# Performance work log

Hardware: AMD Instinct MI355X
Metric: run time of the kernel (lower is better)

Reference implementation:

```python
import jax, jax.numpy as jnp
import numpy as np

H, D, IN, E, N = 4, 16, 64, 400000, 100000
RELS = [("c1c1", "C1", "C1"), ("c1c2", "C1", "C2"), ("c1c3", "C1", "C3"),
        ("c2c1", "C2", "C1"), ("c2c2", "C2", "C2"), ("c2c3", "C2", "C3"),
        ("c3c1", "C3", "C1"), ("c3c2", "C3", "C2"), ("c3c3", "C3", "C3")]
TYPES = ("C1", "C2", "C3")


def setup_inputs() -> dict:
    key = jax.random.key(0)
    ks = iter(jax.random.split(key, 128))
    inp = {}
    for t in TYPES:
        inp["feat_" + t] = jax.random.normal(next(ks), (N, IN), jnp.float32)
        inp["W_" + t] = jax.random.normal(next(ks), (IN, H * D), jnp.float32) * 0.05
        inp["b_" + t] = jnp.zeros((H * D,), jnp.float32)
    for r, s, d in RELS:
        inp["W_" + r] = jax.random.normal(next(ks), (IN, H * D), jnp.float32) * 0.05
        inp["b_" + r] = jnp.zeros((H * D,), jnp.float32)
        inp["asrc_" + r] = jax.random.normal(next(ks), (H, D), jnp.float32) * 0.1
        inp["adst_" + r] = jax.random.normal(next(ks), (H, D), jnp.float32) * 0.1
        inp["src_" + r] = jax.random.randint(next(ks), (E,), 0, N, jnp.int32)
        inp["dst_" + r] = jax.random.randint(next(ks), (E,), 0, N, jnp.int32)
    return inp


def _forward(feats, selfp, relp):
    # leaky_relu with negative_slope = l_alpha = 0.2
    lrelu = lambda x: jnp.where(x >= 0, x, 0.2 * x)
    # per-type self projections Wh_T  [N, H, D]
    Wh_self = {t: (feats[t] @ selfp[t][0] + selfp[t][1]).reshape(-1, H, D) for t in TYPES}
    agg = {t: jnp.zeros((feats[t].shape[0], H, D), feats[t].dtype) for t in TYPES}
    for r, s, d in RELS:
        W, b, asrc, adst, src, dst = relp[r]
        # project once per source node, then gather per edge (same math as per-edge fc)
        Wh = (feats[s] @ W + b).reshape(-1, H, D)      # [Ns, H, D]
        whe = Wh[src]                                   # [E, H, D]
        # attention logits: (Wh_e * a_src).sum(-1) + (Wh_self_dst * a_dst).sum(-1)
        e = lrelu((whe * asrc).sum(-1) + (Wh_self[d][dst] * adst).sum(-1))  # [E, H]
        # nn.Softmax(dim=1) in the original acts over the heads axis of [E, H, 1]
        alpha = jax.nn.softmax(e, axis=1)[..., None]    # [E, H, 1]
        agg[d] = agg[d] + jax.ops.segment_sum(whe * alpha, dst, num_segments=agg[d].shape[0])
    return tuple(jax.nn.relu(agg[t]) for t in TYPES)


def reference(feat_C1, feat_C2, feat_C3, W_C1, b_C1, W_C2, b_C2, W_C3, b_C3,
              W_c1c1, b_c1c1, asrc_c1c1, adst_c1c1, src_c1c1, dst_c1c1,
              W_c1c2, b_c1c2, asrc_c1c2, adst_c1c2, src_c1c2, dst_c1c2,
              W_c1c3, b_c1c3, asrc_c1c3, adst_c1c3, src_c1c3, dst_c1c3,
              W_c2c1, b_c2c1, asrc_c2c1, adst_c2c1, src_c2c1, dst_c2c1,
              W_c2c2, b_c2c2, asrc_c2c2, adst_c2c2, src_c2c2, dst_c2c2,
              W_c2c3, b_c2c3, asrc_c2c3, adst_c2c3, src_c2c3, dst_c2c3,
              W_c3c1, b_c3c1, asrc_c3c1, adst_c3c1, src_c3c1, dst_c3c1,
              W_c3c2, b_c3c2, asrc_c3c2, adst_c3c2, src_c3c2, dst_c3c2,
              W_c3c3, b_c3c3, asrc_c3c3, adst_c3c3, src_c3c3, dst_c3c3):
    L = dict(locals())
    feats = {t: L["feat_" + t] for t in TYPES}
    selfp = {t: (L["W_" + t], L["b_" + t]) for t in TYPES}
    relp = {r: (L["W_" + r], L["b_" + r], L["asrc_" + r], L["adst_" + r], L["src_" + r], L["dst_" + r]) for r, _, _ in RELS}
    return _forward(feats, selfp, relp)
```

## Files before the change

kernel.cpp:

```cpp
#include <hip/hip_runtime.h>
#include <hip/hip_bf16.h>

constexpr int IN_F = 64;
constexpr int HD   = 64;

constexpr int BW_BITS = 10;
constexpr int BWIDTH  = 1 << BW_BITS;
constexpr int BCAP    = 6144;
constexpr int BIN_EPT = 16;
constexpr int BIN_CHUNK = 256 * BIN_EPT;

constexpr int PROJ_ROWS  = 128;
constexpr int LDS_STRIDE = 72;
constexpr int NJOBS      = 18;

typedef __attribute__((ext_vector_type(8))) short short8;
typedef __attribute__((ext_vector_type(4))) float floatx4;
typedef __attribute__((ext_vector_type(4))) unsigned short us4;
typedef __attribute__((ext_vector_type(8))) unsigned short us8;

static __device__ __forceinline__ float bf2f(unsigned short u) {
  union { unsigned int i; float f; } c; c.i = ((unsigned int)u) << 16; return c.f;
}
static __device__ __forceinline__ unsigned short f2bf_bits(float f) {
  union { __hip_bfloat16 h; unsigned short u; } c; c.h = __float2bfloat16(f); return c.u;
}

struct PrepParams {
  const float* W[3][4];
  const float* b[3][4];
  const float* asrc[9];
  const float* adst[9];
  unsigned short* Bpack;
  float* biasPack;
  unsigned* bcnt;
  int nbc;
};

__global__ __launch_bounds__(64) void prep_kernel(PrepParams pp) {
  const int t = blockIdx.x / NJOBS;
  const int j = blockIdx.x % NJOBS;
  const int lane = threadIdx.x;
  const int q = lane >> 4, n = lane & 15;

  {
    const int gid = blockIdx.x * 64 + lane;
    if (gid < pp.nbc) pp.bcnt[gid] = 0u;
  }

  const float* W; const float* bv; const float* av = nullptr;
  int n0 = 0; bool dotjob;
  if (j < 3) {
    W = pp.W[t][0]; bv = pp.b[t][0]; av = pp.adst[j * 3 + t]; dotjob = true;
  } else {
    const int jj = j - 3, p = jj / 5, sub = jj % 5;
    W = pp.W[t][1 + p]; bv = pp.b[t][1 + p];
    if (sub < 4) { n0 = sub * 16; dotjob = false; }
    else { av = pp.asrc[t * 3 + p]; dotjob = true; }
  }

  unsigned short* outB = pp.Bpack + (size_t)(t * NJOBS + j) * 2 * 64 * 8;
  for (int kt = 0; kt < 2; ++kt) {
    for (int jj = 0; jj < 8; ++jj) {
      const int k = kt * 32 + q * 8 + jj;
      float v = 0.f;
      if (!dotjob) v = W[k * 64 + n0 + n];
      else if (n < 4) {
        for (int d = 0; d < 16; ++d) v += W[k * 64 + n * 16 + d] * av[n * 16 + d];
      }
      outB[(kt * 64 + lane) * 8 + jj] = f2bf_bits(v);
    }
  }
  if (lane < 16) {
    float v = 0.f;
    if (!dotjob) v = bv[n0 + lane];
    else if (lane < 4) {
      for (int d = 0; d < 16; ++d) v += bv[lane * 16 + d] * av[lane * 16 + d];
    }
    pp.biasPack[(t * NJOBS + j) * 16 + lane] = v;
  }
}

struct ProjParams {
  const float* feat[3];
  const unsigned short* Bpack;
  const float* biasPack;
  unsigned short* wh[9];
  float* sdot[9];
  float* ddot[9];
  int N;
};

static __device__ __forceinline__ void proj_body(const ProjParams& p, int bx, int t,
                                                 unsigned short* featL) {
  const int n0blk = bx * PROJ_ROWS;
  const int tid = threadIdx.x;
  const int N = p.N;

  {
    const float* feat = p.feat[t];
    #pragma unroll
    for (int c = 0; c < 8; ++c) {
      const int flat = c * 256 + tid;
      const int row = flat >> 4;
      const int c4  = (flat & 15) << 2;
      const int gr = n0blk + row;
      float4 v = make_float4(0.f, 0.f, 0.f, 0.f);
      if (gr < N) v = *(const float4*)(feat + (size_t)gr * IN_F + c4);
      ushort4 o;
      o.x = f2bf_bits(v.x); o.y = f2bf_bits(v.y);
      o.z = f2bf_bits(v.z); o.w = f2bf_bits(v.w);
      *(ushort4*)(featL + row * LDS_STRIDE + c4) = o;
    }
  }
  __syncthreads();

  const int wave = tid >> 6;
  const int lane = tid & 63;
  const int q = lane >> 4, l15 = lane & 15;

  short8 afrag[2][2];
  #pragma unroll
  for (int mt = 0; mt < 2; ++mt) {
    const int row = wave * 32 + mt * 16 + l15;
    #pragma unroll
    for (int kt = 0; kt < 2; ++kt) {
      afrag[mt][kt] = *(const short8*)(featL + row * LDS_STRIDE + kt * 32 + q * 8);
    }
  }
  __syncthreads();

  const unsigned short* Bbase = p.Bpack + (size_t)t * NJOBS * 2 * 64 * 8;
  const float* biasBase = p.biasPack + (size_t)t * NJOBS * 16;

  short8 b0 = *(const short8*)(Bbase + 0 * 512 + lane * 8);
  short8 b1 = *(const short8*)(Bbase + 1 * 512 + lane * 8);
  float bias = biasBase[l15];

  for (int j = 0; j < NJOBS; ++j) {
    short8 b0n, b1n; float biasn = 0.f;
    if (j + 1 < NJOBS) {
      b0n = *(const short8*)(Bbase + ((size_t)(j + 1) * 2 + 0) * 512 + lane * 8);
      b1n = *(const short8*)(Bbase + ((size_t)(j + 1) * 2 + 1) * 512 + lane * 8);
      biasn = biasBase[(j + 1) * 16 + l15];
    }

    #pragma unroll
    for (int mt = 0; mt < 2; ++mt) {
      floatx4 acc = {bias, bias, bias, bias};
      acc = __builtin_amdgcn_mfma_f32_16x16x32_bf16(afrag[mt][0], b0, acc, 0, 0, 0);
      acc = __builtin_amdgcn_mfma_f32_16x16x32_bf16(afrag[mt][1], b1, acc, 0, 0, 0);
      const int lrbase = wave * 32 + mt * 16 + q * 4;
      if (j < 3) {
        if (l15 < 4) {
          float* dp = p.ddot[j * 3 + t];
          #pragma unroll
          for (int r = 0; r < 4; ++r) {
            const int gr = n0blk + lrbase + r;
            if (gr < N) dp[(size_t)gr * 4 + l15] = acc[r];
          }
        }
      } else {
        const int jj = j - 3, pidx = jj / 5, sub = jj % 5, ri = t * 3 + pidx;
        if (sub < 4) {
          #pragma unroll
          for (int r = 0; r < 4; ++r) {
            featL[(lrbase + r) * LDS_STRIDE + sub * 16 + l15] = f2bf_bits(acc[r]);
          }
        } else if (l15 < 4) {
          float* sp = p.sdot[ri];
          #pragma unroll
          for (int r = 0; r < 4; ++r) {
            const int gr = n0blk + lrbase + r;
            if (gr < N) sp[(size_t)gr * 4 + l15] = acc[r];
          }
        }
      }
    }

    if (j >= 3 && ((j - 3) % 5) == 3) {
      const int ri = t * 3 + (j - 3) / 5;
      unsigned short* whp = p.wh[ri];
      const int lr = wave * 32 + (lane >> 1);
      const int gr = n0blk + lr;
      const int c0 = (lane & 1) * 32;
      if (gr < N) {
        #pragma unroll
        for (int k2 = 0; k2 < 4; ++k2) {
          us8 v = *(const us8*)(featL + lr * LDS_STRIDE + c0 + k2 * 8);
          *(us8*)(whp + (size_t)gr * HD + c0 + k2 * 8) = v;
        }
      }
    }

    b0 = b0n; b1 = b1n; bias = biasn;
  }
}

struct EdgeLists { const int* src[9]; const int* dst[9]; int E; int N; };

static __device__ __forceinline__ void bin_body(const EdgeLists& el, unsigned* bcnt,
                                                unsigned* binBuf, int nbuck,
                                                int bx, int r, unsigned* ldsu) {
  unsigned* bh    = ldsu;
  unsigned* bcur  = ldsu + 128;
  unsigned* bbase = ldsu + 256;
  const int tid = threadIdx.x;
  const int e0  = bx * BIN_CHUNK;
  const int E   = el.E;
  const int* srcp = el.src[r];
  const int* dstp = el.dst[r];

  if (tid < 128) { bh[tid] = 0u; bcur[tid] = 0u; }
  __syncthreads();

  int sv[BIN_EPT], dv[BIN_EPT];
  #pragma unroll
  for (int i = 0; i < BIN_EPT; ++i) {
    const int e = e0 + i * 256 + tid;
    if (e < E) {
      sv[i] = srcp[e];
      dv[i] = dstp[e];
      atomicAdd(&bh[dv[i] >> BW_BITS], 1u);
    } else dv[i] = -1;
  }
  __syncthreads();

  if (tid < 128) {
    bbase[tid] = (tid < nbuck && bh[tid] > 0u)
                   ? atomicAdd(bcnt + (size_t)r * nbuck + tid, bh[tid]) : 0u;
  }
  __syncthreads();

  unsigned* bb = binBuf + (size_t)r * nbuck * BCAP;
  #pragma unroll
  for (int i = 0; i < BIN_EPT; ++i) {
    if (dv[i] >= 0) {
      const int b = dv[i] >> BW_BITS;
      const unsigned pos = bbase[b] + atomicAdd(&bcur[b], 1u);
      if (pos < (unsigned)BCAP)
        bb[(size_t)b * BCAP + pos] = (unsigned)sv[i] | ((unsigned)(dv[i] & (BWIDTH - 1)) << 17);
    }
  }
}

struct FusedParams {
  ProjParams proj;
  EdgeLists el;
  unsigned* bcnt;
  unsigned* binBuf;
  int nbuck;
  int projNB;
  int binNB;
};

__global__ __launch_bounds__(256) void fused_kernel(FusedParams fp) {
  __shared__ unsigned short ldsBuf[PROJ_ROWS * LDS_STRIDE];
  const int projTotal = fp.projNB * 3;
  const int bid = (int)blockIdx.x;
  if (bid < projTotal) {
    proj_body(fp.proj, bid % fp.projNB, bid / fp.projNB, ldsBuf);
  } else {
    const int b2 = bid - projTotal;
    bin_body(fp.el, fp.bcnt, fp.binBuf, fp.nbuck,
             b2 % fp.binNB, b2 / fp.binNB, (unsigned*)ldsBuf);
  }
}

struct CsrParams {
  const unsigned* binBuf;
  const unsigned* bcnt;
  unsigned* offsets;
  unsigned* perm;
  unsigned short* alf;
  const float* sdot[9];
  const float* ddot[9];
  int N, E, nbuck;
};

__global__ __launch_bounds__(256) void csr_kernel(CsrParams cp) {
  const int r   = blockIdx.y;
  const int b   = blockIdx.x;
  const int tid = threadIdx.x;
  const int N = cp.N, E = cp.E, nbuck = cp.nbuck;
  const unsigned* bcr = cp.bcnt + (size_t)r * nbuck;
  unsigned* offr = cp.offsets + (size_t)r * (N + 1);
  unsigned* permr = cp.perm + (size_t)r * E;
  unsigned short* alfr = cp.alf + (size_t)r * E * 4;
  const float* sdr = cp.sdot[r];
  const float* ddr = cp.ddot[r];

  __shared__ unsigned S[BWIDTH];
  __shared__ unsigned T[256];
  __shared__ unsigned permL[BCAP];

  unsigned pre = (tid < b) ? bcr[tid] : 0u;
  if (pre > (unsigned)BCAP) pre = BCAP;
  pre += __shfl_xor(pre, 1);  pre += __shfl_xor(pre, 2);
  pre += __shfl_xor(pre, 4);  pre += __shfl_xor(pre, 8);
  pre += __shfl_xor(pre, 16); pre += __shfl_xor(pre, 32);
  if ((tid & 63) == 0) T[tid >> 6] = pre;
  unsigned cnt = bcr[b];
  if (cnt > (unsigned)BCAP) cnt = BCAP;
  __syncthreads();
  const unsigned base = T[0] + T[1] + T[2] + T[3];
  __syncthreads();

  const unsigned* buf = cp.binBuf + ((size_t)r * nbuck + b) * BCAP;

  for (int i = tid; i < BWIDTH; i += 256) S[i] = 0u;
  __syncthreads();

  for (unsigned i = tid; i < cnt; i += 256) atomicAdd(&S[buf[i] >> 17], 1u);
  __syncthreads();

  const int b4 = tid * 4;
  unsigned loc0 = S[b4], loc1 = S[b4 + 1], loc2 = S[b4 + 2], loc3 = S[b4 + 3];
  unsigned s = loc0 + loc1 + loc2 + loc3;
  T[tid] = s;
  __syncthreads();
  for (int d = 1; d < 256; d <<= 1) {
    const unsigned v = T[tid];
    const unsigned a = (tid >= d) ? T[tid - d] : 0u;
    __syncthreads();
    T[tid] = v + a;
    __syncthreads();
  }
  unsigned run = T[tid] - s;
  S[b4]     = run;  run += loc0;
  S[b4 + 1] = run;  run += loc1;
  S[b4 + 2] = run;  run += loc2;
  S[b4 + 3] = run;
  __syncthreads();

  const int d0 = b * BWIDTH;
  for (int i = tid; i < BWIDTH; i += 256) {
    const int d = d0 + i;
    if (d < N) offr[d] = base + S[i];
  }
  if (b == 0 && tid == 0) offr[N] = (unsigned)E;
  __syncthreads();

  for (unsigned i = tid; i < cnt; i += 256) {
    const unsigned v = buf[i];
    const unsigned pos = atomicAdd(&S[v >> 17], 1u);
    permL[pos] = v;
  }
  __syncthreads();

  for (unsigned i = tid; i < cnt; i += 256) {
    const unsigned v = permL[i];
    const unsigned sv = v & 0x1FFFFu;
    const int dn = d0 + (int)(v >> 17);
    permr[base + i] = sv;

    const float4 sd = *(const float4*)(sdr + (size_t)sv * 4);
    const float4 dd = *(const float4*)(ddr + (size_t)dn * 4);
    float e0 = sd.x + dd.x, e1 = sd.y + dd.y, e2 = sd.z + dd.z, e3 = sd.w + dd.w;
    e0 = (e0 >= 0.f) ? e0 : 0.2f * e0;
    e1 = (e1 >= 0.f) ? e1 : 0.2f * e1;
    e2 = (e2 >= 0.f) ? e2 : 0.2f * e2;
    e3 = (e3 >= 0.f) ? e3 : 0.2f * e3;
    const float m = fmaxf(fmaxf(e0, e1), fmaxf(e2, e3));
    const float x0 = __expf(e0 - m);
    const float x1 = __expf(e1 - m);
    const float x2 = __expf(e2 - m);
    const float x3 = __expf(e3 - m);
    const float inv = 1.f / (x0 + x1 + x2 + x3);
    uint2 packed;
    packed.x = ((unsigned)f2bf_bits(x1 * inv) << 16) | f2bf_bits(x0 * inv);
    packed.y = ((unsigned)f2bf_bits(x3 * inv) << 16) | f2bf_bits(x2 * inv);
    *(uint2*)(alfr + (size_t)(base + i) * 4) = packed;
  }
}

struct AggParams {
  const unsigned* offsets[9];
  const unsigned* perm[9];
  const unsigned short* alf[9];
  const unsigned short* wh[9];
  float* outp[3];
  int N, E;
};

__global__ __launch_bounds__(256) void agg_kernel(AggParams p, int t) {
  const int w    = threadIdx.x >> 6;
  const int lane = threadIdx.x & 63;
  const int n    = blockIdx.x * 4 + w;
  if (n >= p.N) return;
  const int slot = lane >> 3;
  const int l8   = lane & 7;
  const unsigned hb = (unsigned)((l8 >> 1) * 2);

  unsigned st[3], en[3];
  const char* __restrict__ pm[3];
  const char* __restrict__ al[3];
  const char* __restrict__ whr[3];
  #pragma unroll
  for (int sj = 0; sj < 3; ++sj) {
    const int r = sj * 3 + t;
    pm[sj]  = (const char*)p.perm[r];
    al[sj]  = (const char*)p.alf[r];
    whr[sj] = (const char*)p.wh[r];
    st[sj]  = p.offsets[r][n];
    en[sj]  = p.offsets[r][n + 1];
  }

  float acc[8];
  #pragma unroll
  for (int k = 0; k < 8; ++k) acc[k] = 0.f;

  unsigned sv[3]; float a[3];
  #pragma unroll
  for (int sj = 0; sj < 3; ++sj) {
    const unsigned s = st[sj], e = en[sj];
    const unsigned pos = s + (unsigned)slot;
    const unsigned pc  = (e > s) ? ((pos < e) ? pos : e - 1) : 0u;
    sv[sj] = *(const unsigned*)(pm[sj] + pc * 4u);
    a[sj]  = (pos < e) ? bf2f(*(const unsigned short*)(al[sj] + pc * 8u + hb)) : 0.f;
  }

  us8 wv[3];
  #pragma unroll
  for (int sj = 0; sj < 3; ++sj) {
    wv[sj] = *(const us8*)(whr[sj] + sv[sj] * 128u + (unsigned)(l8 * 16));
  }

  #pragma unroll
  for (int sj = 0; sj < 3; ++sj) {
    #pragma unroll
    for (int k = 0; k < 8; ++k) {
      acc[k] = fmaf(a[sj], bf2f(wv[sj][k]), acc[k]);
    }
  }

  #pragma unroll
  for (int sj = 0; sj < 3; ++sj) {
    const unsigned e = en[sj];
    for (unsigned bse = st[sj] + 8; bse < e; bse += 8) {
      const unsigned pos  = bse + (unsigned)slot;
      const unsigned posc = (pos < e) ? pos : e - 1;
      const unsigned s2 = *(const unsigned*)(pm[sj] + posc * 4u);
      const float a2 = (pos < e) ? bf2f(*(const unsigned short*)(al[sj] + posc * 8u + hb)) : 0.f;
      const us8 wv2 = *(const us8*)(whr[sj] + s2 * 128u + (unsigned)(l8 * 16));
      #pragma unroll
      for (int k = 0; k < 8; ++k) {
        acc[k] = fmaf(a2, bf2f(wv2[k]), acc[k]);
      }
    }
  }

  #pragma unroll
  for (int k = 0; k < 8; ++k) {
    acc[k] += __shfl_xor(acc[k], 8);
    acc[k] += __shfl_xor(acc[k], 16);
    acc[k] += __shfl_xor(acc[k], 32);
  }

  if (slot == 0) {
    float4 v0, v1;
    v0.x = fmaxf(acc[0], 0.f); v0.y = fmaxf(acc[1], 0.f);
    v0.z = fmaxf(acc[2], 0.f); v0.w = fmaxf(acc[3], 0.f);
    v1.x = fmaxf(acc[4], 0.f); v1.y = fmaxf(acc[5], 0.f);
    v1.z = fmaxf(acc[6], 0.f); v1.w = fmaxf(acc[7], 0.f);
    float* op = p.outp[t] + (size_t)n * HD + l8 * 8;
    *(float4*)(op) = v0;
    *(float4*)(op + 4) = v1;
  }
}

extern "C" void kernel_launch(void* const* d_in, const int* in_sizes, int n_in,
                              void* d_out, int out_size, void* d_ws, size_t ws_size,
                              hipStream_t stream) {
  const int N = in_sizes[0] / IN_F;
  const int E = in_sizes[9 + 4];
  const int nbuck = (N + BWIDTH - 1) >> BW_BITS;

  FusedParams fp; AggParams ap; CsrParams cp; PrepParams qq;
  ProjParams& pp = fp.proj;
  EdgeLists& el = fp.el;
  pp.N = N; ap.N = N; ap.E = E; el.E = E; el.N = N;
  cp.N = N; cp.E = E; cp.nbuck = nbuck;

  for (int t = 0; t < 3; ++t) {
    pp.feat[t] = (const float*)d_in[t * 3 + 0];
    qq.W[t][0] = (const float*)d_in[t * 3 + 1];
    qq.b[t][0] = (const float*)d_in[t * 3 + 2];
    for (int j = 0; j < 3; ++j) {
      const int base = 9 + (t * 3 + j) * 6;
      qq.W[t][1 + j] = (const float*)d_in[base + 0];
      qq.b[t][1 + j] = (const float*)d_in[base + 1];
    }
  }

  char* ws = (char*)d_ws;
  const size_t whBytes  = (size_t)N * HD * sizeof(__hip_bfloat16);
  const size_t dotBytes = (size_t)N * 4 * sizeof(float);
  char* whBase   = ws;
  char* sdotBase = whBase + 9 * whBytes;
  char* ddotBase = sdotBase + 9 * dotBytes;
  unsigned* offsets = (unsigned*)(ddotBase + 9 * dotBytes);
  unsigned* bcnt    = offsets + (size_t)9 * (N + 1);
  unsigned* perm    = bcnt + (size_t)9 * ((nbuck + 63) & ~63);
  unsigned short* alf = (unsigned short*)(perm + (size_t)9 * E);
  unsigned* binBuf  = (unsigned*)(alf + (size_t)9 * E * 4);
  unsigned short* Bpack = (unsigned short*)(binBuf + (size_t)9 * nbuck * BCAP);
  float* biasPack = (float*)(Bpack + (size_t)3 * NJOBS * 2 * 64 * 8);

  cp.offsets = offsets; cp.perm = perm; cp.alf = alf;
  cp.binBuf = binBuf; cp.bcnt = bcnt;
  qq.Bpack = Bpack; qq.biasPack = biasPack;
  qq.bcnt = bcnt; qq.nbc = 9 * nbuck;
  pp.Bpack = Bpack; pp.biasPack = biasPack;
  fp.bcnt = bcnt; fp.binBuf = binBuf; fp.nbuck = nbuck;
  fp.projNB = (N + PROJ_ROWS - 1) / PROJ_ROWS;
  fp.binNB  = (E + BIN_CHUNK - 1) / BIN_CHUNK;

  for (int ri = 0; ri < 9; ++ri) {
    const int base = 9 + ri * 6;
    qq.asrc[ri] = (const float*)d_in[base + 2];
    qq.adst[ri] = (const float*)d_in[base + 3];
    pp.wh[ri]   = (unsigned short*)(whBase + (size_t)ri * whBytes);
    pp.sdot[ri] = (float*)(sdotBase + (size_t)ri * dotBytes);
    pp.ddot[ri] = (float*)(ddotBase + (size_t)ri * dotBytes);
    el.src[ri]  = (const int*)d_in[base + 4];
    el.dst[ri]  = (const int*)d_in[base + 5];
    cp.sdot[ri] = pp.sdot[ri];
    cp.ddot[ri] = pp.ddot[ri];
    ap.wh[ri]   = pp.wh[ri];
    ap.alf[ri]  = alf + (size_t)ri * E * 4;
    ap.offsets[ri] = offsets + (size_t)ri * (N + 1);
    ap.perm[ri]    = perm + (size_t)ri * E;
  }
  for (int t = 0; t < 3; ++t) ap.outp[t] = (float*)d_out + (size_t)t * N * HD;

  prep_kernel<<<dim3(3 * NJOBS), 64, 0, stream>>>(qq);

  const int nblk = fp.projNB * 3 + fp.binNB * 9;
  fused_kernel<<<dim3(nblk), 256, 0, stream>>>(fp);

  csr_kernel<<<dim3(nbuck, 9), 256, 0, stream>>>(cp);

  for (int t = 0; t < 3; ++t)
    agg_kernel<<<dim3((N + 3) / 4), 256, 0, stream>>>(ap, t);
}
```

Measured before the change: 557.2 us.

## Replace CSR build and per-node aggregation with bucketed LDS-atomic aggregation

Destination buckets shrink to 64 nodes and are shared by the three relations that feed each destination type. The relation index is packed into the binned edge word. A new fab kernel computes the per-edge head softmax and accumulates alpha-weighted projected features into a shared-memory tile with LDS float atomics, then writes the ReLU output. This drops the CSR offset/permutation pass, the global perm and alpha buffers, and three separate aggregation launches. In exchange it relies on LDS atomics and a fixed per-bucket capacity of 1280 edges, which silently drops any overflow.

```diff
diff --git a/kernel.cpp b/kernel.cpp
--- a/kernel.cpp
+++ b/kernel.cpp
@@ -4,11 +4,12 @@
 constexpr int IN_F = 64;
 constexpr int HD   = 64;
 
-constexpr int BW_BITS = 10;
+constexpr int BW_BITS = 6;
 constexpr int BWIDTH  = 1 << BW_BITS;
-constexpr int BCAP    = 6144;
+constexpr int FBCAP   = 1280;
 constexpr int BIN_EPT = 16;
 constexpr int BIN_CHUNK = 256 * BIN_EPT;
+constexpr int ACC_PAD  = 66;
 
 constexpr int PROJ_ROWS  = 128;
 constexpr int LDS_STRIDE = 72;
@@ -16,7 +17,6 @@
 
 typedef __attribute__((ext_vector_type(8))) short short8;
 typedef __attribute__((ext_vector_type(4))) float floatx4;
-typedef __attribute__((ext_vector_type(4))) unsigned short us4;
 typedef __attribute__((ext_vector_type(8))) unsigned short us8;
 
 static __device__ __forceinline__ float bf2f(unsigned short u) {
@@ -43,10 +43,8 @@
   const int lane = threadIdx.x;
   const int q = lane >> 4, n = lane & 15;
 
-  {
-    const int gid = blockIdx.x * 64 + lane;
-    if (gid < pp.nbc) pp.bcnt[gid] = 0u;
-  }
+  for (int gid = blockIdx.x * 64 + lane; gid < pp.nbc; gid += 64 * gridDim.x)
+    pp.bcnt[gid] = 0u;
 
   const float* W; const float* bv; const float* av = nullptr;
   int n0 = 0; bool dotjob;
@@ -201,17 +199,19 @@
 
 static __device__ __forceinline__ void bin_body(const EdgeLists& el, unsigned* bcnt,
                                                 unsigned* binBuf, int nbuck,
-                                                int bx, int r, unsigned* ldsu) {
+                                                int bx, int ri, unsigned* ldsu) {
   unsigned* bh    = ldsu;
-  unsigned* bcur  = ldsu + 128;
-  unsigned* bbase = ldsu + 256;
+  unsigned* bcur  = ldsu + nbuck;
+  unsigned* bbase = ldsu + 2 * nbuck;
   const int tid = threadIdx.x;
   const int e0  = bx * BIN_CHUNK;
   const int E   = el.E;
-  const int* srcp = el.src[r];
-  const int* dstp = el.dst[r];
-
-  if (tid < 128) { bh[tid] = 0u; bcur[tid] = 0u; }
+  const int tt  = ri % 3;
+  const int sj  = ri / 3;
+  const int* srcp = el.src[ri];
+  const int* dstp = el.dst[ri];
+
+  for (int i = tid; i < nbuck; i += 256) { bh[i] = 0u; bcur[i] = 0u; }
   __syncthreads();
 
   int sv[BIN_EPT], dv[BIN_EPT];
@@ -226,20 +226,22 @@
   }
   __syncthreads();
 
-  if (tid < 128) {
-    bbase[tid] = (tid < nbuck && bh[tid] > 0u)
-                   ? atomicAdd(bcnt + (size_t)r * nbuck + tid, bh[tid]) : 0u;
-  }
-  __syncthreads();
-
-  unsigned* bb = binBuf + (size_t)r * nbuck * BCAP;
+  for (int i = tid; i < nbuck; i += 256) {
+    bbase[i] = (bh[i] > 0u)
+                 ? atomicAdd(bcnt + (size_t)tt * nbuck + i, bh[i]) : 0u;
+  }
+  __syncthreads();
+
+  unsigned* bb = binBuf + (size_t)tt * nbuck * FBCAP;
   #pragma unroll
   for (int i = 0; i < BIN_EPT; ++i) {
     if (dv[i] >= 0) {
       const int b = dv[i] >> BW_BITS;
       const unsigned pos = bbase[b] + atomicAdd(&bcur[b], 1u);
-      if (pos < (unsigned)BCAP)
-        bb[(size_t)b * BCAP + pos] = (unsigned)sv[i] | ((unsigned)(dv[i] & (BWIDTH - 1)) << 17);
+      if (pos < (unsigned)FBCAP)
+        bb[(size_t)b * FBCAP + pos] =
+          (unsigned)sv[i] | ((unsigned)(dv[i] & (BWIDTH - 1)) << 17)
+                          | ((unsigned)sj << 23);
     }
   }
 }
@@ -255,217 +257,118 @@
 };
 
 __global__ __launch_bounds__(256) void fused_kernel(FusedParams fp) {
-  __shared__ unsigned short ldsBuf[PROJ_ROWS * LDS_STRIDE];
+  __shared__ unsigned ldsU[4704];
   const int projTotal = fp.projNB * 3;
   const int bid = (int)blockIdx.x;
   if (bid < projTotal) {
-    proj_body(fp.proj, bid % fp.projNB, bid / fp.projNB, ldsBuf);
+    proj_body(fp.proj, bid % fp.projNB, bid / fp.projNB, (unsigned short*)ldsU);
   } else {
     const int b2 = bid - projTotal;
     bin_body(fp.el, fp.bcnt, fp.binBuf, fp.nbuck,
-             b2 % fp.binNB, b2 / fp.binNB, (unsigned*)ldsBuf);
-  }
-}
-
-struct CsrParams {
+             b2 % fp.binNB, b2 / fp.binNB, ldsU);
+  }
+}
+
+struct FabParams {
+  const unsigned* bcnt;
   const unsigned* binBuf;
-  const unsigned* bcnt;
-  unsigned* offsets;
-  unsigned* perm;
-  unsigned short* alf;
   const float* sdot[9];
   const float* ddot[9];
-  int N, E, nbuck;
-};
-
-__global__ __launch_bounds__(256) void csr_kernel(CsrParams cp) {
-  const int r   = blockIdx.y;
-  const int b   = blockIdx.x;
-  const int tid = threadIdx.x;
-  const int N = cp.N, E = cp.E, nbuck = cp.nbuck;
-  const unsigned* bcr = cp.bcnt + (size_t)r * nbuck;
-  unsigned* offr = cp.offsets + (size_t)r * (N + 1);
-  unsigned* permr = cp.perm + (size_t)r * E;
-  unsigned short* alfr = cp.alf + (size_t)r * E * 4;
-  const float* sdr = cp.sdot[r];
-  const float* ddr = cp.ddot[r];
-
-  __shared__ unsigned S[BWIDTH];
-  __shared__ unsigned T[256];
-  __shared__ unsigned permL[BCAP];
-
-  unsigned pre = (tid < b) ? bcr[tid] : 0u;
-  if (pre > (unsigned)BCAP) pre = BCAP;
-  pre += __shfl_xor(pre, 1);  pre += __shfl_xor(pre, 2);
-  pre += __shfl_xor(pre, 4);  pre += __shfl_xor(pre, 8);
-  pre += __shfl_xor(pre, 16); pre += __shfl_xor(pre, 32);
-  if ((tid & 63) == 0) T[tid >> 6] = pre;
-  unsigned cnt = bcr[b];
-  if (cnt > (unsigned)BCAP) cnt = BCAP;
-  __syncthreads();
-  const unsigned base = T[0] + T[1] + T[2] + T[3];
-  __syncthreads();
-
-  const unsigned* buf = cp.binBuf + ((size_t)r * nbuck + b) * BCAP;
-
-  for (int i = tid; i < BWIDTH; i += 256) S[i] = 0u;
-  __syncthreads();
-
-  for (unsigned i = tid; i < cnt; i += 256) atomicAdd(&S[buf[i] >> 17], 1u);
-  __syncthreads();
-
-  const int b4 = tid * 4;
-  unsigned loc0 = S[b4], loc1 = S[b4 + 1], loc2 = S[b4 + 2], loc3 = S[b4 + 3];
-  unsigned s = loc0 + loc1 + loc2 + loc3;
-  T[tid] = s;
-  __syncthreads();
-  for (int d = 1; d < 256; d <<= 1) {
-    const unsigned v = T[tid];
-    const unsigned a = (tid >= d) ? T[tid - d] : 0u;
-    __syncthreads();
-    T[tid] = v + a;
-    __syncthreads();
-  }
-  unsigned run = T[tid] - s;
-  S[b4]     = run;  run += loc0;
-  S[b4 + 1] = run;  run += loc1;
-  S[b4 + 2] = run;  run += loc2;
-  S[b4 + 3] = run;
-  __syncthreads();
-
-  const int d0 = b * BWIDTH;
-  for (int i = tid; i < BWIDTH; i += 256) {
-    const int d = d0 + i;
-    if (d < N) offr[d] = base + S[i];
-  }
-  if (b == 0 && tid == 0) offr[N] = (unsigned)E;
-  __syncthreads();
-
-  for (unsigned i = tid; i < cnt; i += 256) {
-    const unsigned v = buf[i];
-    const unsigned pos = atomicAdd(&S[v >> 17], 1u);
-    permL[pos] = v;
-  }
-  __syncthreads();
-
-  for (unsigned i = tid; i < cnt; i += 256) {
-    const unsigned v = permL[i];
-    const unsigned sv = v & 0x1FFFFu;
-    const int dn = d0 + (int)(v >> 17);
-    permr[base + i] = sv;
-
-    const float4 sd = *(const float4*)(sdr + (size_t)sv * 4);
-    const float4 dd = *(const float4*)(ddr + (size_t)dn * 4);
-    float e0 = sd.x + dd.x, e1 = sd.y + dd.y, e2 = sd.z + dd.z, e3 = sd.w + dd.w;
-    e0 = (e0 >= 0.f) ? e0 : 0.2f * e0;
-    e1 = (e1 >= 0.f) ? e1 : 0.2f * e1;
-    e2 = (e2 >= 0.f) ? e2 : 0.2f * e2;
-    e3 = (e3 >= 0.f) ? e3 : 0.2f * e3;
-    const float m = fmaxf(fmaxf(e0, e1), fmaxf(e2, e3));
-    const float x0 = __expf(e0 - m);
-    const float x1 = __expf(e1 - m);
-    const float x2 = __expf(e2 - m);
-    const float x3 = __expf(e3 - m);
-    const float inv = 1.f / (x0 + x1 + x2 + x3);
-    uint2 packed;
-    packed.x = ((unsigned)f2bf_bits(x1 * inv) << 16) | f2bf_bits(x0 * inv);
-    packed.y = ((unsigned)f2bf_bits(x3 * inv) << 16) | f2bf_bits(x2 * inv);
-    *(uint2*)(alfr + (size_t)(base + i) * 4) = packed;
-  }
-}
-
-struct AggParams {
-  const unsigned* offsets[9];
-  const unsigned* perm[9];
-  const unsigned short* alf[9];
   const unsigned short* wh[9];
   float* outp[3];
-  int N, E;
+  int N, nbuck;
 };
 
-__global__ __launch_bounds__(256) void agg_kernel(AggParams p, int t) {
-  const int w    = threadIdx.x >> 6;
-  const int lane = threadIdx.x & 63;
-  const int n    = blockIdx.x * 4 + w;
-  if (n >= p.N) return;
-  const int slot = lane >> 3;
-  const int l8   = lane & 7;
-  const unsigned hb = (unsigned)((l8 >> 1) * 2);
-
-  unsigned st[3], en[3];
-  const char* __restrict__ pm[3];
-  const char* __restrict__ al[3];
-  const char* __restrict__ whr[3];
-  #pragma unroll
-  for (int sj = 0; sj < 3; ++sj) {
-    const int r = sj * 3 + t;
-    pm[sj]  = (const char*)p.perm[r];
-    al[sj]  = (const char*)p.alf[r];
-    whr[sj] = (const char*)p.wh[r];
-    st[sj]  = p.offsets[r][n];
-    en[sj]  = p.offsets[r][n + 1];
-  }
-
-  float acc[8];
-  #pragma unroll
-  for (int k = 0; k < 8; ++k) acc[k] = 0.f;
-
-  unsigned sv[3]; float a[3];
-  #pragma unroll
-  for (int sj = 0; sj < 3; ++sj) {
-    const unsigned s = st[sj], e = en[sj];
-    const unsigned pos = s + (unsigned)slot;
-    const unsigned pc  = (e > s) ? ((pos < e) ? pos : e - 1) : 0u;
-    sv[sj] = *(const unsigned*)(pm[sj] + pc * 4u);
-    a[sj]  = (pos < e) ? bf2f(*(const unsigned short*)(al[sj] + pc * 8u + hb)) : 0.f;
-  }
-
-  us8 wv[3];
-  #pragma unroll
-  for (int sj = 0; sj < 3; ++sj) {
-    wv[sj] = *(const us8*)(whr[sj] + sv[sj] * 128u + (unsigned)(l8 * 16));
-  }
-
-  #pragma unroll
-  for (int sj = 0; sj < 3; ++sj) {
-    #pragma unroll
-    for (int k = 0; k < 8; ++k) {
-      acc[k] = fmaf(a[sj], bf2f(wv[sj][k]), acc[k]);
-    }
-  }
-
-  #pragma unroll
-  for (int sj = 0; sj < 3; ++sj) {
-    const unsigned e = en[sj];
-    for (unsigned bse = st[sj] + 8; bse < e; bse += 8) {
-      const unsigned pos  = bse + (unsigned)slot;
-      const unsigned posc = (pos < e) ? pos : e - 1;
-      const unsigned s2 = *(const unsigned*)(pm[sj] + posc * 4u);
-      const float a2 = (pos < e) ? bf2f(*(const unsigned short*)(al[sj] + posc * 8u + hb)) : 0.f;
-      const us8 wv2 = *(const us8*)(whr[sj] + s2 * 128u + (unsigned)(l8 * 16));
+__global__ __launch_bounds__(256) void fab_kernel(FabParams fb) {
+  const int t  = blockIdx.y;
+  const int b  = blockIdx.x;
+  const int d0 = b * BWIDTH;
+  const int tid = threadIdx.x;
+  const int N = fb.N;
+
+  __shared__ float accum[BWIDTH][ACC_PAD];
+  __shared__ float ddL[3][BWIDTH][4];
+  __shared__ float alphaL[256][4];
+  __shared__ unsigned wordL[256];
+
+  for (int i = tid; i < BWIDTH * ACC_PAD; i += 256)
+    (&accum[0][0])[i] = 0.f;
+  if (tid < 3 * BWIDTH) {
+    const int sj = tid >> BW_BITS, i = tid & (BWIDTH - 1);
+    const int d = d0 + i;
+    float4 v = make_float4(0.f, 0.f, 0.f, 0.f);
+    if (d < N) v = *(const float4*)(fb.ddot[sj * 3 + t] + (size_t)d * 4);
+    ddL[sj][i][0] = v.x; ddL[sj][i][1] = v.y;
+    ddL[sj][i][2] = v.z; ddL[sj][i][3] = v.w;
+  }
+  __syncthreads();
+
+  unsigned cnt = fb.bcnt[(size_t)t * fb.nbuck + b];
+  if (cnt > (unsigned)FBCAP) cnt = FBCAP;
+  const unsigned* buf = fb.binBuf + ((size_t)t * fb.nbuck + b) * FBCAP;
+
+  const int l8 = tid & 7;
+  const int eslot = tid >> 3;
+  const int h = l8 >> 1;
+
+  for (unsigned c0 = 0; c0 < cnt; c0 += 256) {
+    const unsigned lim = (cnt - c0 < 256u) ? (cnt - c0) : 256u;
+
+    if (tid < (int)lim) {
+      const unsigned v  = buf[c0 + tid];
+      const unsigned sv = v & 0x1FFFFu;
+      const unsigned dl = (v >> 17) & (BWIDTH - 1);
+      const unsigned sj = v >> 23;
+      const float4 sd = *(const float4*)(fb.sdot[sj * 3 + t] + (size_t)sv * 4);
+      float e0 = sd.x + ddL[sj][dl][0];
+      float e1 = sd.y + ddL[sj][dl][1];
+      float e2 = sd.z + ddL[sj][dl][2];
+      float e3 = sd.w + ddL[sj][dl][3];
+      e0 = (e0 >= 0.f) ? e0 : 0.2f * e0;
+      e1 = (e1 >= 0.f) ? e1 : 0.2f * e1;
+      e2 = (e2 >= 0.f) ? e2 : 0.2f * e2;
+      e3 = (e3 >= 0.f) ? e3 : 0.2f * e3;
+      const float m = fmaxf(fmaxf(e0, e1), fmaxf(e2, e3));
+      const float x0 = __expf(e0 - m);
+      const float x1 = __expf(e1 - m);
+      const float x2 = __expf(e2 - m);
+      const float x3 = __expf(e3 - m);
+      const float inv = 1.f / (x0 + x1 + x2 + x3);
+      alphaL[tid][0] = x0 * inv; alphaL[tid][1] = x1 * inv;
+      alphaL[tid][2] = x2 * inv; alphaL[tid][3] = x3 * inv;
+      wordL[tid] = v;
+    }
+    __syncthreads();
+
+    for (unsigned j = (unsigned)eslot; j < lim; j += 32) {
+      const unsigned v  = wordL[j];
+      const unsigned sv = v & 0x1FFFFu;
+      const unsigned dl = (v >> 17) & (BWIDTH - 1);
+      const unsigned sj = v >> 23;
+      const float a = alphaL[j][h];
+      const us8 wv = *(const us8*)((const char*)fb.wh[sj * 3 + t]
+                                   + sv * 128u + (unsigned)(l8 * 16));
+      float* ar = &accum[dl][l8 * 8];
       #pragma unroll
-      for (int k = 0; k < 8; ++k) {
-        acc[k] = fmaf(a2, bf2f(wv2[k]), acc[k]);
-      }
-    }
-  }
-
-  #pragma unroll
-  for (int k = 0; k < 8; ++k) {
-    acc[k] += __shfl_xor(acc[k], 8);
-    acc[k] += __shfl_xor(acc[k], 16);
-    acc[k] += __shfl_xor(acc[k], 32);
-  }
-
-  if (slot == 0) {
-    float4 v0, v1;
-    v0.x = fmaxf(acc[0], 0.f); v0.y = fmaxf(acc[1], 0.f);
-    v0.z = fmaxf(acc[2], 0.f); v0.w = fmaxf(acc[3], 0.f);
-    v1.x = fmaxf(acc[4], 0.f); v1.y = fmaxf(acc[5], 0.f);
-    v1.z = fmaxf(acc[6], 0.f); v1.w = fmaxf(acc[7], 0.f);
-    float* op = p.outp[t] + (size_t)n * HD + l8 * 8;
-    *(float4*)(op) = v0;
-    *(float4*)(op + 4) = v1;
+      for (int k = 0; k < 8; ++k)
+        atomicAdd(&ar[k], a * bf2f(wv[k]));
+    }
+    __syncthreads();
+  }
+
+  float* op = fb.outp[t];
+  for (int f4 = tid; f4 < BWIDTH * 16; f4 += 256) {
+    const int row = f4 >> 4;
+    const int c4  = (f4 & 15) << 2;
+    const int d = d0 + row;
+    if (d < N) {
+      float4 o;
+      o.x = fmaxf(accum[row][c4 + 0], 0.f);
+      o.y = fmaxf(accum[row][c4 + 1], 0.f);
+      o.z = fmaxf(accum[row][c4 + 2], 0.f);
+      o.w = fmaxf(accum[row][c4 + 3], 0.f);
+      *(float4*)(op + (size_t)d * HD + c4) = o;
+    }
   }
 }
 
@@ -476,11 +379,11 @@
   const int E = in_sizes[9 + 4];
   const int nbuck = (N + BWIDTH - 1) >> BW_BITS;
 
-  FusedParams fp; AggParams ap; CsrParams cp; PrepParams qq;
+  FusedParams fp; FabParams fb; PrepParams qq;
   ProjParams& pp = fp.proj;
   EdgeLists& el = fp.el;
-  pp.N = N; ap.N = N; ap.E = E; el.E = E; el.N = N;
-  cp.N = N; cp.E = E; cp.nbuck = nbuck;
+  pp.N = N; el.E = E; el.N = N;
+  fb.N = N; fb.nbuck = nbuck;
 
   for (int t = 0; t < 3; ++t) {
     pp.feat[t] = (const float*)d_in[t * 3 + 0];
@@ -499,22 +402,18 @@
   char* whBase   = ws;
   char* sdotBase = whBase + 9 * whBytes;
   char* ddotBase = sdotBase + 9 * dotBytes;
-  unsigned* offsets = (unsigned*)(ddotBase + 9 * dotBytes);
-  unsigned* bcnt    = offsets + (size_t)9 * (N + 1);
-  unsigned* perm    = bcnt + (size_t)9 * ((nbuck + 63) & ~63);
-  unsigned short* alf = (unsigned short*)(perm + (size_t)9 * E);
-  unsigned* binBuf  = (unsigned*)(alf + (size_t)9 * E * 4);
-  unsigned short* Bpack = (unsigned short*)(binBuf + (size_t)9 * nbuck * BCAP);
+  unsigned* bcnt   = (unsigned*)(ddotBase + 9 * dotBytes);
+  unsigned* binBuf = bcnt + (((size_t)3 * nbuck + 63) & ~(size_t)63);
+  unsigned short* Bpack = (unsigned short*)(binBuf + (size_t)3 * nbuck * FBCAP);
   float* biasPack = (float*)(Bpack + (size_t)3 * NJOBS * 2 * 64 * 8);
 
-  cp.offsets = offsets; cp.perm = perm; cp.alf = alf;
-  cp.binBuf = binBuf; cp.bcnt = bcnt;
   qq.Bpack = Bpack; qq.biasPack = biasPack;
-  qq.bcnt = bcnt; qq.nbc = 9 * nbuck;
+  qq.bcnt = bcnt; qq.nbc = 3 * nbuck;
   pp.Bpack = Bpack; pp.biasPack = biasPack;
   fp.bcnt = bcnt; fp.binBuf = binBuf; fp.nbuck = nbuck;
   fp.projNB = (N + PROJ_ROWS - 1) / PROJ_ROWS;
   fp.binNB  = (E + BIN_CHUNK - 1) / BIN_CHUNK;
+  fb.bcnt = bcnt; fb.binBuf = binBuf;
 
   for (int ri = 0; ri < 9; ++ri) {
     const int base = 9 + ri * 6;
@@ -525,22 +424,16 @@
     pp.ddot[ri] = (float*)(ddotBase + (size_t)ri * dotBytes);
     el.src[ri]  = (const int*)d_in[base + 4];
     el.dst[ri]  = (const int*)d_in[base + 5];
-    cp.sdot[ri] = pp.sdot[ri];
-    cp.ddot[ri] = pp.ddot[ri];
-    ap.wh[ri]   = pp.wh[ri];
-    ap.alf[ri]  = alf + (size_t)ri * E * 4;
-    ap.offsets[ri] = offsets + (size_t)ri * (N + 1);
-    ap.perm[ri]    = perm + (size_t)ri * E;
-  }
-  for (int t = 0; t < 3; ++t) ap.outp[t] = (float*)d_out + (size_t)t * N * HD;
+    fb.sdot[ri] = pp.sdot[ri];
+    fb.ddot[ri] = pp.ddot[ri];
+    fb.wh[ri]   = pp.wh[ri];
+  }
+  for (int t = 0; t < 3; ++t) fb.outp[t] = (float*)d_out + (size_t)t * N * HD;
 
   prep_kernel<<<dim3(3 * NJOBS), 64, 0, stream>>>(qq);
 
   const int nblk = fp.projNB * 3 + fp.binNB * 9;
   fused_kernel<<<dim3(nblk), 256, 0, stream>>>(fp);
 
-  csr_kernel<<<dim3(nbuck, 9), 256, 0, stream>>>(cp);
-
-  for (int t = 0; t < 3; ++t)
-    agg_kernel<<<dim3((N + 3) / 4), 256, 0, stream>>>(ap, t);
-}
+  fab_kernel<<<dim3(nbuck, 3), 256, 0, stream>>>(fb);
+}
```

Result: slower. 1.550 ms (+178.2%).
